# Performance work log

Hardware: AMD Instinct MI355X
Metric: run time of the kernel (lower is better)

The kernel has to match this reference:

```python
import jax, jax.numpy as jnp
import numpy as np

N = 50000   # nodes (subjects in population graph)
E = 800000  # edges (similarity graph, avg degree 16)
F = 128     # node features


def setup_inputs() -> dict:
    key = jax.random.key(0)
    ks = jax.random.split(key, 8)

    def glorot(k, shape):
        scale = 1.0 / np.sqrt(shape[0])
        return jax.random.normal(k, shape, jnp.float32) * scale

    x = jax.random.normal(ks[0], (N, F), jnp.float32)
    edge_index = jax.random.randint(ks[1], (2, E), 0, N, dtype=jnp.int64)
    return {
        "x": x,
        "edge_index": edge_index,
        "W1": glorot(ks[2], (F, 128)),   "b1": jnp.zeros((128,), jnp.float32),
        "W2": glorot(ks[3], (128, 64)),  "b2": jnp.zeros((64,), jnp.float32),
        "Wf1": glorot(ks[4], (64, 32)),  "bf1": jnp.zeros((32,), jnp.float32),
        "Wf2": glorot(ks[5], (32, 1)),   "bf2": jnp.zeros((1,), jnp.float32),
    }


def reference(x, edge_index, W1, b1, W2, b2, Wf1, bf1, Wf2, bf2):
    n = x.shape[0]
    # GCNConv (PyG default): add self-loops, symmetric deg^{-1/2} normalization
    loops = jnp.arange(n, dtype=edge_index.dtype)
    src = jnp.concatenate([edge_index[0], loops])  # [E+N]
    dst = jnp.concatenate([edge_index[1], loops])  # [E+N]
    deg = jax.ops.segment_sum(jnp.ones_like(dst, x.dtype), dst, num_segments=n)
    dinv = deg ** -0.5  # deg >= 1 thanks to self-loops
    norm = (dinv[src] * dinv[dst])[:, None]  # [E+N, 1]

    def gcn_conv(h, W, b):
        h = h @ W                                    # transform [n, out]
        msg = h[src] * norm                          # gather + normalize
        agg = jax.ops.segment_sum(msg, dst, num_segments=n)  # scatter-add
        return agg + b

    h = jnp.tanh(gcn_conv(x, W1, b1))
    h = jnp.tanh(gcn_conv(h, W2, b2))
    h = jnp.tanh(h @ Wf1 + bf1)
    return h @ Wf2 + bf2  # [n, 1] brain-age prediction
```

## Files before the change

kernel.cpp:

```cpp
#include <hip/hip_runtime.h>
#include <hip/hip_fp16.h>
#include <math.h>

#define TPB 256
#define CAP 64
#define BSHIFT 7
#define BSPAN 128
#define NBLK 256

typedef int   nt_i4 __attribute__((ext_vector_type(4)));
typedef unsigned nt_u4 __attribute__((ext_vector_type(4)));
typedef _Float16 f16x8 __attribute__((ext_vector_type(8)));
typedef float f32x4 __attribute__((ext_vector_type(4)));

__global__ __launch_bounds__(TPB) void detect_dtype(const int* __restrict__ e,
                                                    int* __restrict__ flag) {
  __shared__ int found;
  if (threadIdx.x == 0) found = 0;
  __syncthreads();
  int nz = 0;
  for (int i = threadIdx.x; i < 2048; i += TPB)
    nz |= (e[2 * i + 1] != 0) ? 1 : 0;
  if (nz) atomicOr(&found, 1);
  __syncthreads();
  if (threadIdx.x == 0) *flag = found;
}

__device__ __forceinline__ void load_edge(const void* eptr, int flag, int E,
                                          int e, int& s, int& d) {
  if (flag) {
    const int* p = (const int*)eptr;
    s = p[e];
    d = p[E + e];
  } else {
    const long long* p = (const long long*)eptr;
    s = (int)p[e];
    d = (int)p[E + e];
  }
}

__global__ __launch_bounds__(TPB) void bucket_count(const void* __restrict__ eptr,
                                                    const int* __restrict__ flag,
                                                    int* __restrict__ cnt,
                                                    int E, int nbuck, int chunk) {
  extern __shared__ int hist[];
  const int tid = threadIdx.x;
  const int fl = *flag;
  for (int b = tid; b < nbuck; b += TPB) hist[b] = 0;
  __syncthreads();
  const int start = blockIdx.x * chunk;
  const int end = min(E, start + chunk);
  for (int e = start + tid; e < end; e += TPB) {
    int s, d;
    load_edge(eptr, fl, E, e, s, d);
    atomicAdd(&hist[d >> BSHIFT], 1);
  }
  __syncthreads();
  for (int b = tid; b < nbuck; b += TPB)
    cnt[blockIdx.x * nbuck + b] = hist[b];
}

__global__ __launch_bounds__(TPB) void scan_col(int* __restrict__ cnt,
                                                int* __restrict__ colsum,
                                                int nbuck) {
  __shared__ int buf[TPB];
  const int b = blockIdx.x;
  const int tid = threadIdx.x;
  int v = cnt[tid * nbuck + b];
  buf[tid] = v;
  __syncthreads();
  for (int off = 1; off < TPB; off <<= 1) {
    int t = (tid >= off) ? buf[tid - off] : 0;
    __syncthreads();
    buf[tid] += t;
    __syncthreads();
  }
  cnt[tid * nbuck + b] = buf[tid] - v;
  if (tid == TPB - 1) colsum[b] = buf[tid];
}

__global__ __launch_bounds__(TPB) void scan_bstart(const int* __restrict__ colsum,
                                                   int* __restrict__ bstart,
                                                   int nbuck, int E) {
  __shared__ int buf[TPB];
  __shared__ int carry;
  const int tid = threadIdx.x;
  if (tid == 0) carry = 0;
  __syncthreads();
  for (int base = 0; base < nbuck; base += TPB) {
    int i = base + tid;
    int v = (i < nbuck) ? colsum[i] : 0;
    buf[tid] = v;
    __syncthreads();
    for (int off = 1; off < TPB; off <<= 1) {
      int t = (tid >= off) ? buf[tid - off] : 0;
      __syncthreads();
      buf[tid] += t;
      __syncthreads();
    }
    if (i < nbuck) bstart[i] = carry + buf[tid] - v;
    __syncthreads();
    if (tid == TPB - 1) carry += buf[tid];
    __syncthreads();
  }
  if (tid == 0) bstart[nbuck] = E;
}

__global__ __launch_bounds__(TPB) void bucket_scatter(const void* __restrict__ eptr,
                                                      const int* __restrict__ flag,
                                                      const int* __restrict__ cnt,
                                                      const int* __restrict__ bstart,
                                                      unsigned long long* __restrict__ pairs,
                                                      int E, int nbuck, int chunk) {
  extern __shared__ int cur[];
  const int tid = threadIdx.x;
  const int fl = *flag;
  for (int b = tid; b < nbuck; b += TPB)
    cur[b] = bstart[b] + cnt[blockIdx.x * nbuck + b];
  __syncthreads();
  const int start = blockIdx.x * chunk;
  const int end = min(E, start + chunk);
  for (int e = start + tid; e < end; e += TPB) {
    int s, d;
    load_edge(eptr, fl, E, e, s, d);
    int slot = atomicAdd(&cur[d >> BSHIFT], 1);
    unsigned long long pv = ((unsigned long long)(unsigned)d << 32) | (unsigned)s;
    __builtin_nontemporal_store(pv, &pairs[slot]);
  }
}

__global__ __launch_bounds__(TPB) void ell_build(const unsigned long long* __restrict__ pairs,
                                                 const int* __restrict__ bstart,
                                                 int* __restrict__ ell,
                                                 int* __restrict__ degi,
                                                 float* __restrict__ dinv,
                                                 int n) {
  __shared__ int cnt[BSPAN];
  const int b = blockIdx.x;
  const int tid = threadIdx.x;
  const int base = b << BSHIFT;
  for (int j = tid; j < BSPAN; j += TPB) cnt[j] = 0;
  __syncthreads();
  const int start = bstart[b];
  const int end = bstart[b + 1];
  for (int i = start + tid; i < end; i += TPB) {
    unsigned long long pr = __builtin_nontemporal_load(&pairs[i]);
    int d = (int)(pr >> 32);
    int s = (int)(unsigned)pr;
    int slot = atomicAdd(&cnt[d - base], 1);
    if (slot < CAP) __builtin_nontemporal_store(s, &ell[(size_t)d * CAP + slot]);
  }
  __syncthreads();
  for (int j = tid; j < BSPAN; j += TPB) {
    int node = base + j;
    if (node < n) {
      int c = cnt[j];
      degi[node] = c;
      dinv[node] = rsqrtf((float)(c + 1));
    }
  }
}

template <int NC, typename AT>
__global__ __launch_bounds__(TPB, 4) void gemm_mfma(const AT* __restrict__ A,
                                                    const float* __restrict__ W,
                                                    const float* __restrict__ dinv,
                                                    __half* __restrict__ out, int nrows) {
  constexpr int K = 128;
  constexpr int WT = 136;
  constexpr int NT = NC / 16;
  __shared__ _Float16 Wt[NC * WT];

  const int tid = threadIdx.x;

  for (int idx = tid; idx < NC * (K / 2); idx += TPB) {
    int c = idx % NC;
    int p = idx / NC;
    float w0 = W[(2 * p) * NC + c];
    float w1 = W[(2 * p + 1) * NC + c];
    __half2* dst = (__half2*)&Wt[c * WT + 2 * p];
    *dst = __floats2half2_rn(w0, w1);
  }
  __syncthreads();

  const int w = tid >> 6;
  const int lane = tid & 63;
  const int l15 = lane & 15;
  const int q = lane >> 4;
  const int m_base = blockIdx.x * 64 + w * 16;
  const int m = m_base + l15;
  const bool mok = m < nrows;

  f32x4 acc[NT];
#pragma unroll
  for (int t = 0; t < NT; t++) acc[t] = (f32x4){0.f, 0.f, 0.f, 0.f};

#pragma unroll
  for (int ks = 0; ks < 4; ks++) {
    const int k0 = ks * 32;
    f16x8 a;
    if (sizeof(AT) == 4) {
      float4 f0 = make_float4(0.f, 0.f, 0.f, 0.f), f1 = f0;
      if (mok) {
        const float* ap = (const float*)A + (size_t)m * K + k0 + q * 8;
        f0 = *(const float4*)ap;
        f1 = *(const float4*)(ap + 4);
      }
      a[0] = (_Float16)f0.x; a[1] = (_Float16)f0.y;
      a[2] = (_Float16)f0.z; a[3] = (_Float16)f0.w;
      a[4] = (_Float16)f1.x; a[5] = (_Float16)f1.y;
      a[6] = (_Float16)f1.z; a[7] = (_Float16)f1.w;
    } else {
      union { uint4 u; f16x8 h; } ld;
      ld.u = make_uint4(0, 0, 0, 0);
      if (mok)
        ld.u = *(const uint4*)((const __half*)A + (size_t)m * K + k0 + q * 8);
      a = ld.h;
    }
#pragma unroll
    for (int t = 0; t < NT; t++) {
      f16x8 b = *(const f16x8*)&Wt[(t * 16 + l15) * WT + k0 + q * 8];
      acc[t] = __builtin_amdgcn_mfma_f32_16x16x32_f16(a, b, acc[t], 0, 0, 0);
    }
  }

#pragma unroll
  for (int r = 0; r < 4; r++) {
    int row = m_base + q * 4 + r;
    if (row >= nrows) continue;
    float di = dinv[row];
#pragma unroll
    for (int t = 0; t < NT; t++)
      out[(size_t)row * NC + t * 16 + l15] = (__half)(acc[t][r] * di);
  }
}

__global__ __launch_bounds__(TPB) void gcn_aggregate128(const int* __restrict__ degi,
                                                        const int* __restrict__ ell,
                                                        const __half* __restrict__ t,
                                                        const float* __restrict__ dinv,
                                                        const float* __restrict__ bias,
                                                        __half* __restrict__ h, int n) {
  constexpr int NC = 128, LPN = 16, CPL = 8, NPB = TPB / LPN;
  int tid = threadIdx.x;
  int node = blockIdx.x * NPB + tid / LPN;
  int lane = tid % LPN;
  if (node >= n) return;

  int deg = degi[node];
  if (deg > CAP) deg = CAP;
  const int* nbr = &ell[(size_t)node * CAP];
  const __half* tp = t + (size_t)lane * CPL;

  float acc[CPL];
#pragma unroll
  for (int c = 0; c < CPL; c++) acc[c] = 0.f;

  union Ld { uint4 u4; __half2 h[4]; };
  auto addv = [&](const Ld& v) {
#pragma unroll
    for (int c = 0; c < 4; c++) {
      float2 f = __half22float2(v.h[c]);
      acc[2 * c] += f.x;
      acc[2 * c + 1] += f.y;
    }
  };

  int j = 0;
  for (; j + 8 <= deg; j += 8) {
    nt_i4 n0 = __builtin_nontemporal_load((const nt_i4*)&nbr[j]);
    nt_i4 n1 = __builtin_nontemporal_load((const nt_i4*)&nbr[j + 4]);
    Ld v0, v1, v2, v3, v4, v5, v6, v7;
    v0.u4 = *(const uint4*)&tp[(size_t)n0.x * NC];
    v1.u4 = *(const uint4*)&tp[(size_t)n0.y * NC];
    v2.u4 = *(const uint4*)&tp[(size_t)n0.z * NC];
    v3.u4 = *(const uint4*)&tp[(size_t)n0.w * NC];
    v4.u4 = *(const uint4*)&tp[(size_t)n1.x * NC];
    v5.u4 = *(const uint4*)&tp[(size_t)n1.y * NC];
    v6.u4 = *(const uint4*)&tp[(size_t)n1.z * NC];
    v7.u4 = *(const uint4*)&tp[(size_t)n1.w * NC];
    addv(v0); addv(v1); addv(v2); addv(v3);
    addv(v4); addv(v5); addv(v6); addv(v7);
  }
  for (; j + 4 <= deg; j += 4) {
    nt_i4 n0 = __builtin_nontemporal_load((const nt_i4*)&nbr[j]);
    Ld v0, v1, v2, v3;
    v0.u4 = *(const uint4*)&tp[(size_t)n0.x * NC];
    v1.u4 = *(const uint4*)&tp[(size_t)n0.y * NC];
    v2.u4 = *(const uint4*)&tp[(size_t)n0.z * NC];
    v3.u4 = *(const uint4*)&tp[(size_t)n0.w * NC];
    addv(v0); addv(v1); addv(v2); addv(v3);
  }
  for (; j < deg; j++) {
    Ld v;
    v.u4 = *(const uint4*)&tp[(size_t)nbr[j] * NC];
    addv(v);
  }
  {
    Ld v;
    v.u4 = *(const uint4*)&tp[(size_t)node * NC];
    addv(v);
  }

  float di = dinv[node];
  const float* bp = &bias[lane * CPL];
  float bv[CPL];
#pragma unroll
  for (int c = 0; c < CPL; c += 4) {
    float4 b = *(const float4*)&bp[c];
    bv[c] = b.x; bv[c + 1] = b.y; bv[c + 2] = b.z; bv[c + 3] = b.w;
  }
  union { __half2 hh[4]; nt_u4 u; } o;
#pragma unroll
  for (int c = 0; c < CPL; c += 2)
    o.hh[c / 2] = __float22half2_rn(make_float2(tanhf(acc[c] * di + bv[c]),
                                                tanhf(acc[c + 1] * di + bv[c + 1])));
  __builtin_nontemporal_store(o.u, (nt_u4*)&h[(size_t)node * NC + lane * CPL]);
}

__global__ __launch_bounds__(TPB) void gcn_aggregate_head(
    const int* __restrict__ degi, const int* __restrict__ ell,
    const __half* __restrict__ t, const float* __restrict__ dinv,
    const float* __restrict__ b2, const float* __restrict__ Wf1,
    const float* __restrict__ bf1, const float* __restrict__ Wf2,
    const float* __restrict__ bf2, float* __restrict__ out, int n) {
  constexpr int NC = 64, LPN = 16, NPB = TPB / LPN;
  __shared__ float hrow[NPB][68];
  __shared__ float Wf1s[64 * 32];
  __shared__ float Wf2s[32];
  const int tid = threadIdx.x;

#pragma unroll
  for (int i = 0; i < 2; i++) {
    int lid = tid + i * TPB;
    *(float4*)&Wf1s[lid * 4] = *(const float4*)&Wf1[lid * 4];
  }
  if (tid < 32) Wf2s[tid] = Wf2[tid];

  const int g = tid / LPN;
  const int ll = tid % LPN;
  const int node = blockIdx.x * NPB + g;
  const bool active = node < n;

  float acc[4] = {0.f, 0.f, 0.f, 0.f};
  if (active) {
    int deg = degi[node];
    if (deg > CAP) deg = CAP;
    const int* nbr = &ell[(size_t)node * CAP];
    const __half* tp = t + (size_t)ll * 4;
    union Ld { uint2 u2; __half2 h[2]; };
    auto addv = [&](const Ld& v) {
      float2 f0 = __half22float2(v.h[0]);
      float2 f1 = __half22float2(v.h[1]);
      acc[0] += f0.x; acc[1] += f0.y; acc[2] += f1.x; acc[3] += f1.y;
    };
    int j = 0;
    for (; j + 4 <= deg; j += 4) {
      nt_i4 nn = __builtin_nontemporal_load((const nt_i4*)&nbr[j]);
      Ld v0, v1, v2, v3;
      v0.u2 = *(const uint2*)&tp[(size_t)nn.x * NC];
      v1.u2 = *(const uint2*)&tp[(size_t)nn.y * NC];
      v2.u2 = *(const uint2*)&tp[(size_t)nn.z * NC];
      v3.u2 = *(const uint2*)&tp[(size_t)nn.w * NC];
      addv(v0); addv(v1); addv(v2); addv(v3);
    }
    for (; j < deg; j++) {
      Ld v;
      v.u2 = *(const uint2*)&tp[(size_t)nbr[j] * NC];
      addv(v);
    }
    {
      Ld v;
      v.u2 = *(const uint2*)&tp[(size_t)node * NC];
      addv(v);
    }
    float di = dinv[node];
    float4 b = *(const float4*)&b2[ll * 4];
    hrow[g][ll * 4 + 0] = tanhf(acc[0] * di + b.x);
    hrow[g][ll * 4 + 1] = tanhf(acc[1] * di + b.y);
    hrow[g][ll * 4 + 2] = tanhf(acc[2] * di + b.z);
    hrow[g][ll * 4 + 3] = tanhf(acc[3] * di + b.w);
  }
  __syncthreads();

  float hid0 = bf1[ll];
  float hid1 = bf1[ll + 16];
#pragma unroll 8
  for (int i = 0; i < 64; i++) {
    float hv = hrow[g][i];
    hid0 += hv * Wf1s[i * 32 + ll];
    hid1 += hv * Wf1s[i * 32 + ll + 16];
  }
  float p = tanhf(hid0) * Wf2s[ll] + tanhf(hid1) * Wf2s[ll + 16];
  p += __shfl_down(p, 8, 16);
  p += __shfl_down(p, 4, 16);
  p += __shfl_down(p, 2, 16);
  p += __shfl_down(p, 1, 16);
  if (active && ll == 0) out[node] = p + bf2[0];
}

extern "C" void kernel_launch(void* const* d_in, const int* in_sizes, int n_in,
                              void* d_out, int out_size, void* d_ws, size_t ws_size,
                              hipStream_t stream) {
  const float* x   = (const float*)d_in[0];
  const void*  eix = d_in[1];
  const float* W1  = (const float*)d_in[2];
  const float* b1  = (const float*)d_in[3];
  const float* W2  = (const float*)d_in[4];
  const float* b2  = (const float*)d_in[5];
  const float* Wf1 = (const float*)d_in[6];
  const float* bf1 = (const float*)d_in[7];
  const float* Wf2 = (const float*)d_in[8];
  const float* bf2 = (const float*)d_in[9];
  float* out = (float*)d_out;

  const int N = in_sizes[0] / 128;
  const int E = in_sizes[1] / 2;
  const int nbuck = (N + BSPAN - 1) >> BSHIFT;
  const int chunk = (E + NBLK - 1) / NBLK;
  const size_t histBytes = (size_t)nbuck * 4;

  char* ws = (char*)d_ws;
  size_t off = 0;
  int* degi = (int*)(ws + off); off += (size_t)N * 4;
  float* dinv = (float*)(ws + off); off += (size_t)N * 4;
  int* flag = (int*)(ws + off); off += 64;
  int* cnt = (int*)(ws + off); off += (size_t)NBLK * nbuck * 4;
  int* colsum = (int*)(ws + off); off += (size_t)(nbuck + 4) * 4;
  int* bstart = (int*)(ws + off); off += (size_t)(nbuck + 4) * 4;
  off = (off + 15) & ~(size_t)15;
  unsigned long long* pairs = (unsigned long long*)(ws + off); off += (size_t)E * 8;
  int* ell = (int*)(ws + off); off += (size_t)N * CAP * 4;
  off = (off + 15) & ~(size_t)15;
  __half* t1 = (__half*)(ws + off); off += (size_t)N * 128 * 2;
  __half* h1 = (__half*)(ws + off); off += (size_t)N * 128 * 2;
  __half* t2 = t1;
  (void)ws_size; (void)n_in; (void)out_size;

  detect_dtype<<<1, TPB, 0, stream>>>((const int*)eix, flag);
  bucket_count<<<NBLK, TPB, histBytes, stream>>>(eix, flag, cnt, E, nbuck, chunk);
  scan_col<<<nbuck, TPB, 0, stream>>>(cnt, colsum, nbuck);
  scan_bstart<<<1, TPB, 0, stream>>>(colsum, bstart, nbuck, E);
  bucket_scatter<<<NBLK, TPB, histBytes, stream>>>(eix, flag, cnt, bstart, pairs, E, nbuck, chunk);
  ell_build<<<nbuck, TPB, 0, stream>>>(pairs, bstart, ell, degi, dinv, N);

  gemm_mfma<128, float><<<(N + 63) / 64, TPB, 0, stream>>>(x, W1, dinv, t1, N);
  gcn_aggregate128<<<(N + 15) / 16, TPB, 0, stream>>>(degi, ell, t1, dinv, b1, h1, N);

  gemm_mfma<64, __half><<<(N + 63) / 64, TPB, 0, stream>>>(h1, W2, dinv, t2, N);
  gcn_aggregate_head<<<(N + 15) / 16, TPB, 0, stream>>>(degi, ell, t2, dinv, b2,
                                                        Wf1, bf1, Wf2, bf2, out, N);
}
```

Measured before the change: 235.9 us.

## Replace bucket-sort ELL build with global atomics and fuse layer-2 GEMM into aggregation

```diff
diff --git a/kernel.cpp b/kernel.cpp
--- a/kernel.cpp
+++ b/kernel.cpp
@@ -4,26 +4,29 @@
 
 #define TPB 256
 #define CAP 64
-#define BSHIFT 7
-#define BSPAN 128
-#define NBLK 256
 
 typedef int   nt_i4 __attribute__((ext_vector_type(4)));
 typedef unsigned nt_u4 __attribute__((ext_vector_type(4)));
 typedef _Float16 f16x8 __attribute__((ext_vector_type(8)));
 typedef float f32x4 __attribute__((ext_vector_type(4)));
 
-__global__ __launch_bounds__(TPB) void detect_dtype(const int* __restrict__ e,
-                                                    int* __restrict__ flag) {
-  __shared__ int found;
-  if (threadIdx.x == 0) found = 0;
-  __syncthreads();
-  int nz = 0;
-  for (int i = threadIdx.x; i < 2048; i += TPB)
-    nz |= (e[2 * i + 1] != 0) ? 1 : 0;
-  if (nz) atomicOr(&found, 1);
-  __syncthreads();
-  if (threadIdx.x == 0) *flag = found;
+__global__ __launch_bounds__(TPB) void init_degi(const int* __restrict__ e,
+                                                 int* __restrict__ flag,
+                                                 int* __restrict__ degi, int n) {
+  int i = blockIdx.x * TPB + threadIdx.x;
+  const int stride = gridDim.x * TPB;
+  for (; i < n; i += stride) degi[i] = 0;
+  if (blockIdx.x == 0) {
+    __shared__ int found;
+    if (threadIdx.x == 0) found = 0;
+    __syncthreads();
+    int nz = 0;
+    for (int k = threadIdx.x; k < 2048; k += TPB)
+      nz |= (e[2 * k + 1] != 0) ? 1 : 0;
+    if (nz) atomicOr(&found, 1);
+    __syncthreads();
+    if (threadIdx.x == 0) *flag = found;
+  }
 }
 
 __device__ __forceinline__ void load_edge(const void* eptr, int flag, int E,
@@ -39,124 +42,45 @@
   }
 }
 
-__global__ __launch_bounds__(TPB) void bucket_count(const void* __restrict__ eptr,
-                                                    const int* __restrict__ flag,
-                                                    int* __restrict__ cnt,
-                                                    int E, int nbuck, int chunk) {
-  extern __shared__ int hist[];
-  const int tid = threadIdx.x;
+__global__ __launch_bounds__(TPB) void build_ell(const void* __restrict__ eptr,
+                                                 const int* __restrict__ flag,
+                                                 int* __restrict__ degi,
+                                                 int* __restrict__ ell, int E) {
   const int fl = *flag;
-  for (int b = tid; b < nbuck; b += TPB) hist[b] = 0;
-  __syncthreads();
-  const int start = blockIdx.x * chunk;
-  const int end = min(E, start + chunk);
-  for (int e = start + tid; e < end; e += TPB) {
-    int s, d;
-    load_edge(eptr, fl, E, e, s, d);
-    atomicAdd(&hist[d >> BSHIFT], 1);
-  }
-  __syncthreads();
-  for (int b = tid; b < nbuck; b += TPB)
-    cnt[blockIdx.x * nbuck + b] = hist[b];
-}
-
-__global__ __launch_bounds__(TPB) void scan_col(int* __restrict__ cnt,
-                                                int* __restrict__ colsum,
-                                                int nbuck) {
-  __shared__ int buf[TPB];
-  const int b = blockIdx.x;
-  const int tid = threadIdx.x;
-  int v = cnt[tid * nbuck + b];
-  buf[tid] = v;
-  __syncthreads();
-  for (int off = 1; off < TPB; off <<= 1) {
-    int t = (tid >= off) ? buf[tid - off] : 0;
-    __syncthreads();
-    buf[tid] += t;
-    __syncthreads();
-  }
-  cnt[tid * nbuck + b] = buf[tid] - v;
-  if (tid == TPB - 1) colsum[b] = buf[tid];
-}
-
-__global__ __launch_bounds__(TPB) void scan_bstart(const int* __restrict__ colsum,
-                                                   int* __restrict__ bstart,
-                                                   int nbuck, int E) {
-  __shared__ int buf[TPB];
-  __shared__ int carry;
-  const int tid = threadIdx.x;
-  if (tid == 0) carry = 0;
-  __syncthreads();
-  for (int base = 0; base < nbuck; base += TPB) {
-    int i = base + tid;
-    int v = (i < nbuck) ? colsum[i] : 0;
-    buf[tid] = v;
-    __syncthreads();
-    for (int off = 1; off < TPB; off <<= 1) {
-      int t = (tid >= off) ? buf[tid - off] : 0;
-      __syncthreads();
-      buf[tid] += t;
-      __syncthreads();
-    }
-    if (i < nbuck) bstart[i] = carry + buf[tid] - v;
-    __syncthreads();
-    if (tid == TPB - 1) carry += buf[tid];
-    __syncthreads();
-  }
-  if (tid == 0) bstart[nbuck] = E;
-}
-
-__global__ __launch_bounds__(TPB) void bucket_scatter(const void* __restrict__ eptr,
-                                                      const int* __restrict__ flag,
-                                                      const int* __restrict__ cnt,
-                                                      const int* __restrict__ bstart,
-                                                      unsigned long long* __restrict__ pairs,
-                                                      int E, int nbuck, int chunk) {
-  extern __shared__ int cur[];
-  const int tid = threadIdx.x;
-  const int fl = *flag;
-  for (int b = tid; b < nbuck; b += TPB)
-    cur[b] = bstart[b] + cnt[blockIdx.x * nbuck + b];
-  __syncthreads();
-  const int start = blockIdx.x * chunk;
-  const int end = min(E, start + chunk);
-  for (int e = start + tid; e < end; e += TPB) {
-    int s, d;
-    load_edge(eptr, fl, E, e, s, d);
-    int slot = atomicAdd(&cur[d >> BSHIFT], 1);
-    unsigned long long pv = ((unsigned long long)(unsigned)d << 32) | (unsigned)s;
-    __builtin_nontemporal_store(pv, &pairs[slot]);
-  }
-}
-
-__global__ __launch_bounds__(TPB) void ell_build(const unsigned long long* __restrict__ pairs,
-                                                 const int* __restrict__ bstart,
-                                                 int* __restrict__ ell,
-                                                 int* __restrict__ degi,
-                                                 float* __restrict__ dinv,
-                                                 int n) {
-  __shared__ int cnt[BSPAN];
-  const int b = blockIdx.x;
-  const int tid = threadIdx.x;
-  const int base = b << BSHIFT;
-  for (int j = tid; j < BSPAN; j += TPB) cnt[j] = 0;
-  __syncthreads();
-  const int start = bstart[b];
-  const int end = bstart[b + 1];
-  for (int i = start + tid; i < end; i += TPB) {
-    unsigned long long pr = __builtin_nontemporal_load(&pairs[i]);
-    int d = (int)(pr >> 32);
-    int s = (int)(unsigned)pr;
-    int slot = atomicAdd(&cnt[d - base], 1);
-    if (slot < CAP) __builtin_nontemporal_store(s, &ell[(size_t)d * CAP + slot]);
-  }
-  __syncthreads();
-  for (int j = tid; j < BSPAN; j += TPB) {
-    int node = base + j;
-    if (node < n) {
-      int c = cnt[j];
-      degi[node] = c;
-      dinv[node] = rsqrtf((float)(c + 1));
+  const int t4 = (blockIdx.x * TPB + threadIdx.x) * 4;
+  const int stride = gridDim.x * TPB * 4;
+  for (int e0 = t4; e0 < E; e0 += stride) {
+    if (e0 + 4 <= E) {
+      int s[4], d[4];
+      if (fl) {
+        const int* p = (const int*)eptr;
+        nt_i4 sv = __builtin_nontemporal_load((const nt_i4*)&p[e0]);
+        nt_i4 dv = __builtin_nontemporal_load((const nt_i4*)&p[E + e0]);
+        s[0] = sv.x; s[1] = sv.y; s[2] = sv.z; s[3] = sv.w;
+        d[0] = dv.x; d[1] = dv.y; d[2] = dv.z; d[3] = dv.w;
+      } else {
+        const long long* p = (const long long*)eptr;
+        nt_i4 sa = __builtin_nontemporal_load((const nt_i4*)&p[e0]);
+        nt_i4 sb = __builtin_nontemporal_load((const nt_i4*)&p[e0 + 2]);
+        nt_i4 da = __builtin_nontemporal_load((const nt_i4*)&p[E + e0]);
+        nt_i4 db = __builtin_nontemporal_load((const nt_i4*)&p[E + e0 + 2]);
+        s[0] = sa.x; s[1] = sa.z; s[2] = sb.x; s[3] = sb.z;
+        d[0] = da.x; d[1] = da.z; d[2] = db.x; d[3] = db.z;
+      }
+#pragma unroll
+      for (int j = 0; j < 4; j++) {
+        int slot = atomicAdd(&degi[d[j]], 1);
+        if (slot < CAP)
+          __builtin_nontemporal_store(s[j], &ell[(size_t)d[j] * CAP + slot]);
+      }
+    } else {
+      for (int e = e0; e < E; e++) {
+        int s, d;
+        load_edge(eptr, fl, E, e, s, d);
+        int slot = atomicAdd(&degi[d], 1);
+        if (slot < CAP)
+          __builtin_nontemporal_store(s, &ell[(size_t)d * CAP + slot]);
+      }
     }
   }
 }
@@ -164,7 +88,7 @@
 template <int NC, typename AT>
 __global__ __launch_bounds__(TPB, 4) void gemm_mfma(const AT* __restrict__ A,
                                                     const float* __restrict__ W,
-                                                    const float* __restrict__ dinv,
+                                                    const int* __restrict__ degi,
                                                     __half* __restrict__ out, int nrows) {
   constexpr int K = 128;
   constexpr int WT = 136;
@@ -228,102 +152,138 @@
   for (int r = 0; r < 4; r++) {
     int row = m_base + q * 4 + r;
     if (row >= nrows) continue;
-    float di = dinv[row];
+    float di = rsqrtf((float)(degi[row] + 1));
 #pragma unroll
     for (int t = 0; t < NT; t++)
       out[(size_t)row * NC + t * 16 + l15] = (__half)(acc[t][r] * di);
   }
 }
 
-__global__ __launch_bounds__(TPB) void gcn_aggregate128(const int* __restrict__ degi,
-                                                        const int* __restrict__ ell,
-                                                        const __half* __restrict__ t,
-                                                        const float* __restrict__ dinv,
-                                                        const float* __restrict__ bias,
-                                                        __half* __restrict__ h, int n) {
+__global__ __launch_bounds__(TPB) void gcn_agg1_fused(const int* __restrict__ degi,
+                                                      const int* __restrict__ ell,
+                                                      const __half* __restrict__ t,
+                                                      const float* __restrict__ bias,
+                                                      const float* __restrict__ W2,
+                                                      __half* __restrict__ t2, int n) {
   constexpr int NC = 128, LPN = 16, CPL = 8, NPB = TPB / LPN;
-  int tid = threadIdx.x;
-  int node = blockIdx.x * NPB + tid / LPN;
-  int lane = tid % LPN;
-  if (node >= n) return;
-
-  int deg = degi[node];
-  if (deg > CAP) deg = CAP;
-  const int* nbr = &ell[(size_t)node * CAP];
-  const __half* tp = t + (size_t)lane * CPL;
-
-  float acc[CPL];
-#pragma unroll
-  for (int c = 0; c < CPL; c++) acc[c] = 0.f;
-
-  union Ld { uint4 u4; __half2 h[4]; };
-  auto addv = [&](const Ld& v) {
-#pragma unroll
-    for (int c = 0; c < 4; c++) {
-      float2 f = __half22float2(v.h[c]);
-      acc[2 * c] += f.x;
-      acc[2 * c + 1] += f.y;
-    }
-  };
-
-  int j = 0;
-  for (; j + 8 <= deg; j += 8) {
-    nt_i4 n0 = __builtin_nontemporal_load((const nt_i4*)&nbr[j]);
-    nt_i4 n1 = __builtin_nontemporal_load((const nt_i4*)&nbr[j + 4]);
-    Ld v0, v1, v2, v3, v4, v5, v6, v7;
-    v0.u4 = *(const uint4*)&tp[(size_t)n0.x * NC];
-    v1.u4 = *(const uint4*)&tp[(size_t)n0.y * NC];
-    v2.u4 = *(const uint4*)&tp[(size_t)n0.z * NC];
-    v3.u4 = *(const uint4*)&tp[(size_t)n0.w * NC];
-    v4.u4 = *(const uint4*)&tp[(size_t)n1.x * NC];
-    v5.u4 = *(const uint4*)&tp[(size_t)n1.y * NC];
-    v6.u4 = *(const uint4*)&tp[(size_t)n1.z * NC];
-    v7.u4 = *(const uint4*)&tp[(size_t)n1.w * NC];
-    addv(v0); addv(v1); addv(v2); addv(v3);
-    addv(v4); addv(v5); addv(v6); addv(v7);
-  }
-  for (; j + 4 <= deg; j += 4) {
-    nt_i4 n0 = __builtin_nontemporal_load((const nt_i4*)&nbr[j]);
-    Ld v0, v1, v2, v3;
-    v0.u4 = *(const uint4*)&tp[(size_t)n0.x * NC];
-    v1.u4 = *(const uint4*)&tp[(size_t)n0.y * NC];
-    v2.u4 = *(const uint4*)&tp[(size_t)n0.z * NC];
-    v3.u4 = *(const uint4*)&tp[(size_t)n0.w * NC];
-    addv(v0); addv(v1); addv(v2); addv(v3);
-  }
-  for (; j < deg; j++) {
-    Ld v;
-    v.u4 = *(const uint4*)&tp[(size_t)nbr[j] * NC];
-    addv(v);
-  }
-  {
-    Ld v;
-    v.u4 = *(const uint4*)&tp[(size_t)node * NC];
-    addv(v);
-  }
-
-  float di = dinv[node];
-  const float* bp = &bias[lane * CPL];
-  float bv[CPL];
-#pragma unroll
-  for (int c = 0; c < CPL; c += 4) {
-    float4 b = *(const float4*)&bp[c];
-    bv[c] = b.x; bv[c + 1] = b.y; bv[c + 2] = b.z; bv[c + 3] = b.w;
-  }
-  union { __half2 hh[4]; nt_u4 u; } o;
-#pragma unroll
-  for (int c = 0; c < CPL; c += 2)
-    o.hh[c / 2] = __float22half2_rn(make_float2(tanhf(acc[c] * di + bv[c]),
-                                                tanhf(acc[c + 1] * di + bv[c + 1])));
-  __builtin_nontemporal_store(o.u, (nt_u4*)&h[(size_t)node * NC + lane * CPL]);
+  constexpr int WT = 136;
+  __shared__ _Float16 Wt2[64 * WT];
+  __shared__ _Float16 Ah[NPB * WT];
+
+  const int tid = threadIdx.x;
+
+  for (int idx = tid; idx < 64 * 64; idx += TPB) {
+    int c = idx & 63;
+    int p = idx >> 6;
+    float w0 = W2[(2 * p) * 64 + c];
+    float w1 = W2[(2 * p + 1) * 64 + c];
+    *(__half2*)&Wt2[c * WT + 2 * p] = __floats2half2_rn(w0, w1);
+  }
+
+  const int g = tid / LPN;
+  const int ll = tid % LPN;
+  const int node = blockIdx.x * NPB + g;
+  const bool active = node < n;
+
+  if (active) {
+    int dg = degi[node];
+    float di = rsqrtf((float)(dg + 1));
+    int deg = dg > CAP ? CAP : dg;
+    const int* nbr = &ell[(size_t)node * CAP];
+    const __half* tp = t + (size_t)ll * CPL;
+
+    float acc[CPL];
+#pragma unroll
+    for (int c = 0; c < CPL; c++) acc[c] = 0.f;
+
+    union Ld { uint4 u4; __half2 h[4]; };
+    auto addv = [&](const Ld& v) {
+#pragma unroll
+      for (int c = 0; c < 4; c++) {
+        float2 f = __half22float2(v.h[c]);
+        acc[2 * c] += f.x;
+        acc[2 * c + 1] += f.y;
+      }
+    };
+
+    int j = 0;
+    for (; j + 8 <= deg; j += 8) {
+      nt_i4 n0 = __builtin_nontemporal_load((const nt_i4*)&nbr[j]);
+      nt_i4 n1 = __builtin_nontemporal_load((const nt_i4*)&nbr[j + 4]);
+      Ld v0, v1, v2, v3, v4, v5, v6, v7;
+      v0.u4 = *(const uint4*)&tp[(size_t)n0.x * NC];
+      v1.u4 = *(const uint4*)&tp[(size_t)n0.y * NC];
+      v2.u4 = *(const uint4*)&tp[(size_t)n0.z * NC];
+      v3.u4 = *(const uint4*)&tp[(size_t)n0.w * NC];
+      v4.u4 = *(const uint4*)&tp[(size_t)n1.x * NC];
+      v5.u4 = *(const uint4*)&tp[(size_t)n1.y * NC];
+      v6.u4 = *(const uint4*)&tp[(size_t)n1.z * NC];
+      v7.u4 = *(const uint4*)&tp[(size_t)n1.w * NC];
+      addv(v0); addv(v1); addv(v2); addv(v3);
+      addv(v4); addv(v5); addv(v6); addv(v7);
+    }
+    for (; j + 4 <= deg; j += 4) {
+      nt_i4 n0 = __builtin_nontemporal_load((const nt_i4*)&nbr[j]);
+      Ld v0, v1, v2, v3;
+      v0.u4 = *(const uint4*)&tp[(size_t)n0.x * NC];
+      v1.u4 = *(const uint4*)&tp[(size_t)n0.y * NC];
+      v2.u4 = *(const uint4*)&tp[(size_t)n0.z * NC];
+      v3.u4 = *(const uint4*)&tp[(size_t)n0.w * NC];
+      addv(v0); addv(v1); addv(v2); addv(v3);
+    }
+    for (; j < deg; j++) {
+      Ld v;
+      v.u4 = *(const uint4*)&tp[(size_t)nbr[j] * NC];
+      addv(v);
+    }
+    {
+      Ld v;
+      v.u4 = *(const uint4*)&tp[(size_t)node * NC];
+      addv(v);
+    }
+
+    const float* bp = &bias[ll * CPL];
+    float bv[CPL];
+#pragma unroll
+    for (int c = 0; c < CPL; c += 4) {
+      float4 b = *(const float4*)&bp[c];
+      bv[c] = b.x; bv[c + 1] = b.y; bv[c + 2] = b.z; bv[c + 3] = b.w;
+    }
+    union { _Float16 h[8]; f16x8 v; } o;
+#pragma unroll
+    for (int c = 0; c < CPL; c++)
+      o.h[c] = (_Float16)tanhf(acc[c] * di + bv[c]);
+    *(f16x8*)&Ah[g * WT + ll * CPL] = o.v;
+  }
+  __syncthreads();
+
+  const int w = tid >> 6;
+  const int lane = tid & 63;
+  const int l15 = lane & 15;
+  const int q = lane >> 4;
+  f32x4 acc2 = (f32x4){0.f, 0.f, 0.f, 0.f};
+#pragma unroll
+  for (int ks = 0; ks < 4; ks++) {
+    f16x8 a = *(const f16x8*)&Ah[l15 * WT + ks * 32 + q * 8];
+    f16x8 b = *(const f16x8*)&Wt2[(w * 16 + l15) * WT + ks * 32 + q * 8];
+    acc2 = __builtin_amdgcn_mfma_f32_16x16x32_f16(a, b, acc2, 0, 0, 0);
+  }
+#pragma unroll
+  for (int r = 0; r < 4; r++) {
+    int rn = blockIdx.x * NPB + q * 4 + r;
+    if (rn < n) {
+      float d2 = rsqrtf((float)(degi[rn] + 1));
+      t2[(size_t)rn * 64 + w * 16 + l15] = (__half)(acc2[r] * d2);
+    }
+  }
 }
 
 __global__ __launch_bounds__(TPB) void gcn_aggregate_head(
     const int* __restrict__ degi, const int* __restrict__ ell,
-    const __half* __restrict__ t, const float* __restrict__ dinv,
-    const float* __restrict__ b2, const float* __restrict__ Wf1,
-    const float* __restrict__ bf1, const float* __restrict__ Wf2,
-    const float* __restrict__ bf2, float* __restrict__ out, int n) {
+    const __half* __restrict__ t, const float* __restrict__ b2,
+    const float* __restrict__ Wf1, const float* __restrict__ bf1,
+    const float* __restrict__ Wf2, const float* __restrict__ bf2,
+    float* __restrict__ out, int n) {
   constexpr int NC = 64, LPN = 16, NPB = TPB / LPN;
   __shared__ float hrow[NPB][68];
   __shared__ float Wf1s[64 * 32];
@@ -344,8 +304,9 @@
 
   float acc[4] = {0.f, 0.f, 0.f, 0.f};
   if (active) {
-    int deg = degi[node];
-    if (deg > CAP) deg = CAP;
+    int dg = degi[node];
+    float di = rsqrtf((float)(dg + 1));
+    int deg = dg > CAP ? CAP : dg;
     const int* nbr = &ell[(size_t)node * CAP];
     const __half* tp = t + (size_t)ll * 4;
     union Ld { uint2 u2; __half2 h[2]; };
@@ -355,6 +316,21 @@
       acc[0] += f0.x; acc[1] += f0.y; acc[2] += f1.x; acc[3] += f1.y;
     };
     int j = 0;
+    for (; j + 8 <= deg; j += 8) {
+      nt_i4 n0 = __builtin_nontemporal_load((const nt_i4*)&nbr[j]);
+      nt_i4 n1 = __builtin_nontemporal_load((const nt_i4*)&nbr[j + 4]);
+      Ld v0, v1, v2, v3, v4, v5, v6, v7;
+      v0.u2 = *(const uint2*)&tp[(size_t)n0.x * NC];
+      v1.u2 = *(const uint2*)&tp[(size_t)n0.y * NC];
+      v2.u2 = *(const uint2*)&tp[(size_t)n0.z * NC];
+      v3.u2 = *(const uint2*)&tp[(size_t)n0.w * NC];
+      v4.u2 = *(const uint2*)&tp[(size_t)n1.x * NC];
+      v5.u2 = *(const uint2*)&tp[(size_t)n1.y * NC];
+      v6.u2 = *(const uint2*)&tp[(size_t)n1.z * NC];
+      v7.u2 = *(const uint2*)&tp[(size_t)n1.w * NC];
+      addv(v0); addv(v1); addv(v2); addv(v3);
+      addv(v4); addv(v5); addv(v6); addv(v7);
+    }
     for (; j + 4 <= deg; j += 4) {
       nt_i4 nn = __builtin_nontemporal_load((const nt_i4*)&nbr[j]);
       Ld v0, v1, v2, v3;
@@ -374,7 +350,6 @@
       v.u2 = *(const uint2*)&tp[(size_t)node * NC];
       addv(v);
     }
-    float di = dinv[node];
     float4 b = *(const float4*)&b2[ll * 4];
     hrow[g][ll * 4 + 0] = tanhf(acc[0] * di + b.x);
     hrow[g][ll * 4 + 1] = tanhf(acc[1] * di + b.y);
@@ -416,38 +391,26 @@
 
   const int N = in_sizes[0] / 128;
   const int E = in_sizes[1] / 2;
-  const int nbuck = (N + BSPAN - 1) >> BSHIFT;
-  const int chunk = (E + NBLK - 1) / NBLK;
-  const size_t histBytes = (size_t)nbuck * 4;
 
   char* ws = (char*)d_ws;
   size_t off = 0;
   int* degi = (int*)(ws + off); off += (size_t)N * 4;
-  float* dinv = (float*)(ws + off); off += (size_t)N * 4;
   int* flag = (int*)(ws + off); off += 64;
-  int* cnt = (int*)(ws + off); off += (size_t)NBLK * nbuck * 4;
-  int* colsum = (int*)(ws + off); off += (size_t)(nbuck + 4) * 4;
-  int* bstart = (int*)(ws + off); off += (size_t)(nbuck + 4) * 4;
   off = (off + 15) & ~(size_t)15;
-  unsigned long long* pairs = (unsigned long long*)(ws + off); off += (size_t)E * 8;
   int* ell = (int*)(ws + off); off += (size_t)N * CAP * 4;
   off = (off + 15) & ~(size_t)15;
   __half* t1 = (__half*)(ws + off); off += (size_t)N * 128 * 2;
-  __half* h1 = (__half*)(ws + off); off += (size_t)N * 128 * 2;
-  __half* t2 = t1;
+  __half* t2 = (__half*)(ws + off); off += (size_t)N * 64 * 2;
   (void)ws_size; (void)n_in; (void)out_size;
 
-  detect_dtype<<<1, TPB, 0, stream>>>((const int*)eix, flag);
-  bucket_count<<<NBLK, TPB, histBytes, stream>>>(eix, flag, cnt, E, nbuck, chunk);
-  scan_col<<<nbuck, TPB, 0, stream>>>(cnt, colsum, nbuck);
-  scan_bstart<<<1, TPB, 0, stream>>>(colsum, bstart, nbuck, E);
-  bucket_scatter<<<NBLK, TPB, histBytes, stream>>>(eix, flag, cnt, bstart, pairs, E, nbuck, chunk);
-  ell_build<<<nbuck, TPB, 0, stream>>>(pairs, bstart, ell, degi, dinv, N);
-
-  gemm_mfma<128, float><<<(N + 63) / 64, TPB, 0, stream>>>(x, W1, dinv, t1, N);
-  gcn_aggregate128<<<(N + 15) / 16, TPB, 0, stream>>>(degi, ell, t1, dinv, b1, h1, N);
-
-  gemm_mfma<64, __half><<<(N + 63) / 64, TPB, 0, stream>>>(h1, W2, dinv, t2, N);
-  gcn_aggregate_head<<<(N + 15) / 16, TPB, 0, stream>>>(degi, ell, t2, dinv, b2,
+  init_degi<<<64, TPB, 0, stream>>>((const int*)eix, flag, degi, N);
+  const int bblocks = (E + TPB * 4 - 1) / (TPB * 4);
+  build_ell<<<bblocks, TPB, 0, stream>>>(eix, flag, degi, ell, E);
+
+  gemm_mfma<128, float><<<(N + 63) / 64, TPB, 0, stream>>>(x, W1, degi, t1, N);
+
+  gcn_agg1_fused<<<(N + 15) / 16, TPB, 0, stream>>>(degi, ell, t1, b1, W2, t2, N);
+
+  gcn_aggregate_head<<<(N + 15) / 16, TPB, 0, stream>>>(degi, ell, t2, b2,
                                                         Wf1, bf1, Wf2, bf2, out, N);
 }
```

After: 232.9 us. No clear change (-1.3%).
